# Kernel tuning notes

Measured on AMD Instinct MI355X. Metric: run time of the kernel, lower is better.

Reference implementation:

```python
import jax, jax.numpy as jnp
import numpy as np

B, H, S, D = 2, 16, 2048, 128


def _fp8_roundtrip(x):
    # Simulate fp8 e4m3fnuz storage: values are exactly representable in fp8.
    return x.astype(jnp.float8_e4m3fnuz).astype(jnp.float32)


def setup_inputs() -> dict:
    key = jax.random.key(0)
    k0, k1, k2, k3, k4, k5, k6 = jax.random.split(key, 7)
    q = _fp8_roundtrip(jax.random.normal(k0, (B, H, S, D), jnp.float32))
    k = _fp8_roundtrip(jax.random.normal(k1, (B, H, S, D), jnp.float32))
    v = _fp8_roundtrip(jax.random.normal(k2, (B, H, S, D), jnp.float32))
    # per-tensor dequant scales (positive)
    qs = jax.random.uniform(k3, (1,), jnp.float32, 0.5, 1.5)
    ks = jax.random.uniform(k4, (1,), jnp.float32, 0.5, 1.5)
    vs = jax.random.uniform(k5, (1,), jnp.float32, 0.5, 1.5)
    s = jax.random.normal(k6, (1,), jnp.float32)  # unused by forward (kept for signature fidelity)
    return {"s": s, "q": q, "k": k, "v": v, "qs": qs, "ks": ks, "vs": vs}


def reference(s, q, k, v, qs, ks, vs):
    # Dequantize fp8 tensors with per-tensor scales, then standard SDPA.
    qd = q * qs  # (B,H,S,D)
    kd = k * ks
    vd = v * vs
    scale = 1.0 / np.sqrt(D).astype(np.float32)
    logits = jnp.einsum('bhqd,bhkd->bhqk', qd, kd) * scale  # (B,H,S,S)
    attn = jax.nn.softmax(logits, axis=-1)
    return jnp.einsum('bhqk,bhkd->bhqd', attn, vd)  # (B,H,S,D)
```

## Files before the change

kernel.cpp:

```cpp
#include <hip/hip_runtime.h>


#define S_LEN 2048
#define D_DIM 128
#define BM 128
#define BN 64
#define NT (S_LEN / BN)
#define LDQ 136
#define LDK 136
#define LDP 68
#define LDV 72
#define VROWS 144

typedef _Float16 half8   __attribute__((ext_vector_type(8)));
typedef _Float16 half4_t __attribute__((ext_vector_type(4)));
typedef _Float16 half2_t __attribute__((ext_vector_type(2)));
typedef float    floatx4 __attribute__((ext_vector_type(4)));

__device__ __forceinline__ half8 cvt8(const float4 a, const float4 b) {
    half8 h;
    h[0] = (_Float16)a.x; h[1] = (_Float16)a.y; h[2] = (_Float16)a.z; h[3] = (_Float16)a.w;
    h[4] = (_Float16)b.x; h[5] = (_Float16)b.y; h[6] = (_Float16)b.z; h[7] = (_Float16)b.w;
    return h;
}

__global__ __launch_bounds__(256, 2)
void fa_fwd(const float* __restrict__ qg, const float* __restrict__ kg,
            const float* __restrict__ vg, const float* __restrict__ qsp,
            const float* __restrict__ ksp, const float* __restrict__ vsp,
            float* __restrict__ outg)
{
    __shared__ __align__(16) _Float16 QsPh[BM * LDQ];
    __shared__ __align__(16) _Float16 Ks[BN * LDK];
    __shared__ __align__(16) _Float16 Vt[VROWS * LDV];

    const int tid  = threadIdx.x;
    const int wave = tid >> 6;
    const int lane = tid & 63;
    const int l16  = lane & 15;
    const int quad = lane >> 4;

    const int bid = blockIdx.x;
    const int bh  = ((bid & 7) << 2) + (bid >> 7);
    const int qb  = (bid >> 3) & 15;
    const int q0  = qb * BM;
    const size_t base = (size_t)bh * (S_LEN * D_DIM);

    const float sks    = qsp[0] * ksp[0];
    const float scale  = sks * 0.08838834764831845f;
    const float negM   = -4.0f * sks;
    const float vscale = vsp[0];

    const int c8 = (tid & 15) << 3;
    const int r0 = tid >> 4;
    const int cg = (tid & 31) << 2;
    const int kp0 = tid >> 5;

    const float* kbase = kg + base;
    const float* vbase = vg + base;

    float4 kr[8], vr[8];
    auto load_tile = [&](int kt) {
        const float* kb = kbase + (size_t)(kt * BN) * D_DIM;
        const float* vb = vbase + (size_t)(kt * BN) * D_DIM;
        #pragma unroll
        for (int i = 0; i < 4; ++i) {
            const float* src = kb + (size_t)(r0 + 16 * i) * D_DIM + c8;
            kr[2 * i]     = *(const float4*)src;
            kr[2 * i + 1] = *(const float4*)(src + 4);
        }
        #pragma unroll
        for (int i = 0; i < 4; ++i) {
            const int kp = kp0 + 8 * i;
            vr[2 * i]     = *(const float4*)(vb + (size_t)(2 * kp) * D_DIM + cg);
            vr[2 * i + 1] = *(const float4*)(vb + (size_t)(2 * kp + 1) * D_DIM + cg);
        }
    };
    auto store_tile = [&]() {
        #pragma unroll
        for (int i = 0; i < 4; ++i)
            *(half8*)&Ks[(r0 + 16 * i) * LDK + c8] = cvt8(kr[2 * i], kr[2 * i + 1]);
        #pragma unroll
        for (int i = 0; i < 4; ++i) {
            const int kp = kp0 + 8 * i;
            const float* ap = (const float*)&vr[2 * i];
            const float* bp = (const float*)&vr[2 * i + 1];
            #pragma unroll
            for (int j = 0; j < 4; ++j) {
                const int d  = cg + j;
                const int s  = ((d >> 2) ^ (d >> 5)) & 7;
                const int pb = (kp >> 2) ^ s;
                half2_t h2 = { (_Float16)ap[j], (_Float16)bp[j] };
                *(half2_t*)&Vt[d * LDV + pb * 8 + (kp & 3) * 2] = h2;
            }
        }
    };

    load_tile(0);

    {
        for (int r = r0; r < BM; r += 16) {
            const float* src = qg + base + (size_t)(q0 + r) * D_DIM + c8;
            const float4 f0 = *(const float4*)src;
            const float4 f1 = *(const float4*)(src + 4);
            *(half8*)&QsPh[r * LDQ + c8] = cvt8(f0, f1);
        }
        for (int i = tid; i < (VROWS - D_DIM) * LDV; i += 256)
            Vt[D_DIM * LDV + i] = (i < LDV) ? (_Float16)1.0f : (_Float16)0.0f;
    }
    __syncthreads();

    half8 qf[2][4];
    #pragma unroll
    for (int mf = 0; mf < 2; ++mf)
        #pragma unroll
        for (int d0 = 0; d0 < 4; ++d0)
            qf[mf][d0] = *(const half8*)&QsPh[(wave * 32 + mf * 16 + l16) * LDQ + d0 * 32 + quad * 8];
    _Float16* const Ph = QsPh;

    floatx4 o_acc[2][9];
    #pragma unroll
    for (int mf = 0; mf < 2; ++mf)
        #pragma unroll
        for (int c = 0; c < 9; ++c) o_acc[mf][c] = (floatx4){0.f, 0.f, 0.f, 0.f};

    for (int kt = 0; kt < NT; ++kt) {
        __syncthreads();
        store_tile();
        __syncthreads();
        if (kt + 1 < NT) load_tile(kt + 1);

        floatx4 sacc[2][4];
        #pragma unroll
        for (int mf = 0; mf < 2; ++mf)
            #pragma unroll
            for (int n = 0; n < 4; ++n) sacc[mf][n] = (floatx4){0.f, 0.f, 0.f, 0.f};
        #pragma unroll
        for (int n = 0; n < 4; ++n) {
            #pragma unroll
            for (int d0 = 0; d0 < 4; ++d0) {
                const half8 kf = *(const half8*)&Ks[(n * 16 + l16) * LDK + d0 * 32 + quad * 8];
                sacc[0][n] = __builtin_amdgcn_mfma_f32_16x16x32_f16(qf[0][d0], kf, sacc[0][n], 0, 0, 0);
                sacc[1][n] = __builtin_amdgcn_mfma_f32_16x16x32_f16(qf[1][d0], kf, sacc[1][n], 0, 0, 0);
            }
        }

        #pragma unroll
        for (int mf = 0; mf < 2; ++mf) {
            #pragma unroll
            for (int rg = 0; rg < 4; ++rg) {
                const int prow = (wave * 32 + mf * 16 + quad * 4 + rg) * LDP;
                #pragma unroll
                for (int n = 0; n < 4; ++n) {
                    const float p = __expf(fmaf(sacc[mf][n][rg], scale, negM));
                    Ph[prow + n * 16 + l16] = (_Float16)p;
                }
            }
        }

        #pragma unroll
        for (int k0 = 0; k0 < 2; ++k0) {
            half8 af[2];
            #pragma unroll
            for (int mf = 0; mf < 2; ++mf) {
                const int idx = (wave * 32 + mf * 16 + l16) * LDP + k0 * 32 + quad * 8;
                const half4_t alo = *(const half4_t*)&Ph[idx];
                const half4_t ahi = *(const half4_t*)&Ph[idx + 4];
                af[mf] = (half8){alo[0], alo[1], alo[2], alo[3], ahi[0], ahi[1], ahi[2], ahi[3]};
            }
            #pragma unroll
            for (int c = 0; c < 9; ++c) {
                const int d  = c * 16 + l16;
                const int s  = ((d >> 2) ^ (d >> 5)) & 7;
                const int pb = (k0 * 4 + quad) ^ s;
                const half8 bf = *(const half8*)&Vt[d * LDV + pb * 8];
                o_acc[0][c] = __builtin_amdgcn_mfma_f32_16x16x32_f16(af[0], bf, o_acc[0][c], 0, 0, 0);
                o_acc[1][c] = __builtin_amdgcn_mfma_f32_16x16x32_f16(af[1], bf, o_acc[1][c], 0, 0, 0);
            }
        }
    }

    #pragma unroll
    for (int mf = 0; mf < 2; ++mf) {
        #pragma unroll
        for (int rg = 0; rg < 4; ++rg) {
            const float l    = __shfl(o_acc[mf][8][rg], lane & 48);
            const float invl = vscale / l;
            const int row = q0 + wave * 32 + mf * 16 + quad * 4 + rg;
            float* orow = outg + base + (size_t)row * D_DIM;
            #pragma unroll
            for (int c = 0; c < 8; ++c)
                orow[c * 16 + l16] = o_acc[mf][c][rg] * invl;
        }
    }
}

extern "C" void kernel_launch(void* const* d_in, const int* in_sizes, int n_in,
                              void* d_out, int out_size, void* d_ws, size_t ws_size,
                              hipStream_t stream) {
    const float* q  = (const float*)d_in[1];
    const float* k  = (const float*)d_in[2];
    const float* v  = (const float*)d_in[3];
    const float* qs = (const float*)d_in[4];
    const float* ks = (const float*)d_in[5];
    const float* vs = (const float*)d_in[6];
    float* out = (float*)d_out;

    fa_fwd<<<dim3(512), 256, 0, stream>>>(q, k, v, qs, ks, vs, out);
}
```

Before: 246.9 us.

## Double-buffer K/V shared tiles and permute key order for vectorized P stores

Keeps two shared-memory buffers for K and transposed V, so the next tile is written while the current one is consumed and one barrier per iteration is removed. Loads run two tiles ahead. Keys are permuted consistently between the V transpose layout and the P layout, so each lane writes P as a single half4 and reads it back as half8, and the V XOR swizzle is dropped. Occupancy is lowered to one block per CU because shared memory grows, which risks less latency hiding, and the unswizzled V layout may cause bank conflicts.

Measured after the change: 296.4 us. +20.1%, slower.

```diff
diff --git a/kernel.cpp b/kernel.cpp
--- a/kernel.cpp
+++ b/kernel.cpp
@@ -8,13 +8,12 @@
 #define NT (S_LEN / BN)
 #define LDQ 136
 #define LDK 136
-#define LDP 68
+#define LDP 72
 #define LDV 72
 #define VROWS 144
 
 typedef _Float16 half8   __attribute__((ext_vector_type(8)));
 typedef _Float16 half4_t __attribute__((ext_vector_type(4)));
-typedef _Float16 half2_t __attribute__((ext_vector_type(2)));
 typedef float    floatx4 __attribute__((ext_vector_type(4)));
 
 __device__ __forceinline__ half8 cvt8(const float4 a, const float4 b) {
@@ -24,15 +23,15 @@
     return h;
 }
 
-__global__ __launch_bounds__(256, 2)
+__global__ __launch_bounds__(256, 1)
 void fa_fwd(const float* __restrict__ qg, const float* __restrict__ kg,
             const float* __restrict__ vg, const float* __restrict__ qsp,
             const float* __restrict__ ksp, const float* __restrict__ vsp,
             float* __restrict__ outg)
 {
     __shared__ __align__(16) _Float16 QsPh[BM * LDQ];
-    __shared__ __align__(16) _Float16 Ks[BN * LDK];
-    __shared__ __align__(16) _Float16 Vt[VROWS * LDV];
+    __shared__ __align__(16) _Float16 Ks2[2][BN * LDK];
+    __shared__ __align__(16) _Float16 Vt2[2][VROWS * LDV];
 
     const int tid  = threadIdx.x;
     const int wave = tid >> 6;
@@ -51,10 +50,10 @@
     const float negM   = -4.0f * sks;
     const float vscale = vsp[0];
 
-    const int c8 = (tid & 15) << 3;
-    const int r0 = tid >> 4;
-    const int cg = (tid & 31) << 2;
-    const int kp0 = tid >> 5;
+    const int c8  = (tid & 15) << 3;
+    const int r0  = tid >> 4;
+    const int tq  = tid & 15;
+    const int cg0 = (tid >> 4) << 2;
 
     const float* kbase = kg + base;
     const float* vbase = vg + base;
@@ -70,28 +69,28 @@
             kr[2 * i + 1] = *(const float4*)(src + 4);
         }
         #pragma unroll
-        for (int i = 0; i < 4; ++i) {
-            const int kp = kp0 + 8 * i;
-            vr[2 * i]     = *(const float4*)(vb + (size_t)(2 * kp) * D_DIM + cg);
-            vr[2 * i + 1] = *(const float4*)(vb + (size_t)(2 * kp + 1) * D_DIM + cg);
+        for (int it = 0; it < 2; ++it) {
+            const int cg = cg0 + 64 * it;
+            #pragma unroll
+            for (int u = 0; u < 4; ++u)
+                vr[4 * it + u] = *(const float4*)(vb + (size_t)(tq + 16 * u) * D_DIM + cg);
         }
     };
-    auto store_tile = [&]() {
+    auto store_tile = [&](int b) {
         #pragma unroll
         for (int i = 0; i < 4; ++i)
-            *(half8*)&Ks[(r0 + 16 * i) * LDK + c8] = cvt8(kr[2 * i], kr[2 * i + 1]);
-        #pragma unroll
-        for (int i = 0; i < 4; ++i) {
-            const int kp = kp0 + 8 * i;
-            const float* ap = (const float*)&vr[2 * i];
-            const float* bp = (const float*)&vr[2 * i + 1];
+            *(half8*)&Ks2[b][(r0 + 16 * i) * LDK + c8] = cvt8(kr[2 * i], kr[2 * i + 1]);
+        #pragma unroll
+        for (int it = 0; it < 2; ++it) {
+            const int cg = cg0 + 64 * it;
             #pragma unroll
             for (int j = 0; j < 4; ++j) {
-                const int d  = cg + j;
-                const int s  = ((d >> 2) ^ (d >> 5)) & 7;
-                const int pb = (kp >> 2) ^ s;
-                half2_t h2 = { (_Float16)ap[j], (_Float16)bp[j] };
-                *(half2_t*)&Vt[d * LDV + pb * 8 + (kp & 3) * 2] = h2;
+                const int d = cg + j;
+                half4_t h = { (_Float16)((const float*)&vr[4 * it + 0])[j],
+                              (_Float16)((const float*)&vr[4 * it + 1])[j],
+                              (_Float16)((const float*)&vr[4 * it + 2])[j],
+                              (_Float16)((const float*)&vr[4 * it + 3])[j] };
+                *(half4_t*)&Vt2[b][d * LDV + 4 * tq] = h;
             }
         }
     };
@@ -105,8 +104,11 @@
             const float4 f1 = *(const float4*)(src + 4);
             *(half8*)&QsPh[r * LDQ + c8] = cvt8(f0, f1);
         }
-        for (int i = tid; i < (VROWS - D_DIM) * LDV; i += 256)
-            Vt[D_DIM * LDV + i] = (i < LDV) ? (_Float16)1.0f : (_Float16)0.0f;
+        for (int i = tid; i < (VROWS - D_DIM) * LDV; i += 256) {
+            const _Float16 v = (i < LDV) ? (_Float16)1.0f : (_Float16)0.0f;
+            Vt2[0][D_DIM * LDV + i] = v;
+            Vt2[1][D_DIM * LDV + i] = v;
+        }
     }
     __syncthreads();
 
@@ -118,6 +120,9 @@
             qf[mf][d0] = *(const half8*)&QsPh[(wave * 32 + mf * 16 + l16) * LDQ + d0 * 32 + quad * 8];
     _Float16* const Ph = QsPh;
 
+    store_tile(0);
+    load_tile(1);
+
     floatx4 o_acc[2][9];
     #pragma unroll
     for (int mf = 0; mf < 2; ++mf)
@@ -126,9 +131,11 @@
 
     for (int kt = 0; kt < NT; ++kt) {
         __syncthreads();
-        store_tile();
-        __syncthreads();
-        if (kt + 1 < NT) load_tile(kt + 1);
+        if (kt + 1 < NT) store_tile((kt + 1) & 1);
+        if (kt + 2 < NT) load_tile(kt + 2);
+
+        const _Float16* const Kst = Ks2[kt & 1];
+        const _Float16* const Vtt = Vt2[kt & 1];
 
         floatx4 sacc[2][4];
         #pragma unroll
@@ -139,7 +146,7 @@
         for (int n = 0; n < 4; ++n) {
             #pragma unroll
             for (int d0 = 0; d0 < 4; ++d0) {
-                const half8 kf = *(const half8*)&Ks[(n * 16 + l16) * LDK + d0 * 32 + quad * 8];
+                const half8 kf = *(const half8*)&Kst[(n * 16 + l16) * LDK + d0 * 32 + quad * 8];
                 sacc[0][n] = __builtin_amdgcn_mfma_f32_16x16x32_f16(qf[0][d0], kf, sacc[0][n], 0, 0, 0);
                 sacc[1][n] = __builtin_amdgcn_mfma_f32_16x16x32_f16(qf[1][d0], kf, sacc[1][n], 0, 0, 0);
             }
@@ -149,12 +156,12 @@
         for (int mf = 0; mf < 2; ++mf) {
             #pragma unroll
             for (int rg = 0; rg < 4; ++rg) {
-                const int prow = (wave * 32 + mf * 16 + quad * 4 + rg) * LDP;
+                half4_t ph4;
                 #pragma unroll
-                for (int n = 0; n < 4; ++n) {
-                    const float p = __expf(fmaf(sacc[mf][n][rg], scale, negM));
-                    Ph[prow + n * 16 + l16] = (_Float16)p;
-                }
+                for (int n = 0; n < 4; ++n)
+                    ph4[n] = (_Float16)__expf(fmaf(sacc[mf][n][rg], scale, negM));
+                const int row = wave * 32 + mf * 16 + quad * 4 + rg;
+                *(half4_t*)&Ph[row * LDP + 4 * l16] = ph4;
             }
         }
 
@@ -162,18 +169,12 @@
         for (int k0 = 0; k0 < 2; ++k0) {
             half8 af[2];
             #pragma unroll
-            for (int mf = 0; mf < 2; ++mf) {
-                const int idx = (wave * 32 + mf * 16 + l16) * LDP + k0 * 32 + quad * 8;
-                const half4_t alo = *(const half4_t*)&Ph[idx];
-                const half4_t ahi = *(const half4_t*)&Ph[idx + 4];
-                af[mf] = (half8){alo[0], alo[1], alo[2], alo[3], ahi[0], ahi[1], ahi[2], ahi[3]};
-            }
+            for (int mf = 0; mf < 2; ++mf)
+                af[mf] = *(const half8*)&Ph[(wave * 32 + mf * 16 + l16) * LDP + k0 * 32 + quad * 8];
             #pragma unroll
             for (int c = 0; c < 9; ++c) {
-                const int d  = c * 16 + l16;
-                const int s  = ((d >> 2) ^ (d >> 5)) & 7;
-                const int pb = (k0 * 4 + quad) ^ s;
-                const half8 bf = *(const half8*)&Vt[d * LDV + pb * 8];
+                const int d = c * 16 + l16;
+                const half8 bf = *(const half8*)&Vtt[d * LDV + k0 * 32 + quad * 8];
                 o_acc[0][c] = __builtin_amdgcn_mfma_f32_16x16x32_f16(af[0], bf, o_acc[0][c], 0, 0, 0);
                 o_acc[1][c] = __builtin_amdgcn_mfma_f32_16x16x32_f16(af[1], bf, o_acc[1][c], 0, 0, 0);
             }
```
